# Optimization experiments

Hardware: AMD Instinct MI355X
Metric: run time of the kernel (lower is better)

## Reference

```python
import jax, jax.numpy as jnp
import numpy as np
import math

B, S, D, H, TD = 256, 200, 64, 512, 8


def setup_inputs():
    key = jax.random.key(0)
    ks = jax.random.split(key, 12)
    sd, sh, so = 1.0 / math.sqrt(D), 1.0 / math.sqrt(H), 1.0 / math.sqrt(H + TD)
    return dict(
        x=jax.random.normal(ks[0], (B, S, D), jnp.float32),
        a=jax.random.normal(ks[3], (B, TD), jnp.float32),
        t=jnp.cumsum(jax.random.uniform(ks[2], (B, S), jnp.float32), axis=1),
        mask=(jax.random.uniform(ks[1], (B, S, D)) < 0.8).astype(jnp.float32),
        w_dg_x=jax.random.normal(ks[4], (D,), jnp.float32) * sd,
        b_dg_x=jnp.zeros((D,), jnp.float32),
        W_dg_h=jax.random.normal(ks[5], (H, D), jnp.float32) * sd,
        b_dg_h=jnp.zeros((H,), jnp.float32),
        W=jax.random.normal(ks[6], (3 * H, D), jnp.float32) * sd,
        U=jax.random.normal(ks[7], (3 * H, H), jnp.float32) * sh,
        V=jax.random.normal(ks[8], (3 * H, D), jnp.float32) * sd,
        b=jnp.zeros((3 * H,), jnp.float32),
        attn_v=jnp.ones((H,), jnp.float32),
        W_out=jax.random.normal(ks[9], (H, H + TD), jnp.float32) * so,
        b_out=jnp.zeros((H,), jnp.float32),
    )


def reference(x, a, t, mask, w_dg_x, b_dg_x, W_dg_h, b_dg_h, W, U, V, b, attn_v, W_out, b_out):
    # ---- GRU-D preprocessing: per-feature time gaps delta ----
    x_tm = jnp.transpose(x, (1, 0, 2))    # (S,B,D) time-major
    m_tm = jnp.transpose(mask, (1, 0, 2))
    dt = jnp.diff(t, axis=1, prepend=t[:, :1])      # (B,S), dt[0]=0
    dt_tm = jnp.transpose(dt)[:, :, None]           # (S,B,1)
    # delta[i] = dt[i] + (1 - mask[i-1]) * delta[i-1]; ones at step 0 -> delta[0]=0
    m_prev = jnp.concatenate([jnp.ones((1,) + m_tm.shape[1:], m_tm.dtype), m_tm[:-1]], axis=0)

    def delta_step(d, inp):
        dt_i, mp_i = inp
        d = dt_i + (1.0 - mp_i) * d
        return d, d

    _, delta_tm = jax.lax.scan(delta_step, jnp.zeros((B, D), x.dtype), (dt_tm, m_prev))

    # empirical mean of observed values for imputation
    x_mean = (mask * x).sum((0, 1)) / jnp.maximum(mask.sum((0, 1)), 1.0)  # (D,)

    Wz, Wr, Wh = W[:H], W[H:2 * H], W[2 * H:]
    Uz, Ur, Uh = U[:H], U[H:2 * H], U[2 * H:]
    Vz, Vr, Vh = V[:H], V[H:2 * H], V[2 * H:]
    bz, br, bh = b[:H], b[H:2 * H], b[2 * H:]

    def cell(carry, inp):
        h, x_last = carry
        x_i, m_i, d_i = inp                                        # (B,D) each
        gamma_x = jnp.exp(-jax.nn.relu(w_dg_x * d_i + b_dg_x))     # (B,D) input decay
        gamma_h = jnp.exp(-jax.nn.relu(d_i @ W_dg_h.T + b_dg_h))   # (B,H) hidden decay
        x_hat = m_i * x_i + (1.0 - m_i) * (gamma_x * x_last + (1.0 - gamma_x) * x_mean)
        h_dec = gamma_h * h
        z = jax.nn.sigmoid(x_hat @ Wz.T + h_dec @ Uz.T + m_i @ Vz.T + bz)
        r = jax.nn.sigmoid(x_hat @ Wr.T + h_dec @ Ur.T + m_i @ Vr.T + br)
        h_til = jnp.tanh(x_hat @ Wh.T + (r * h_dec) @ Uh.T + m_i @ Vh.T + bh)
        h_new = (1.0 - z) * h_dec + z * h_til
        x_last_new = m_i * x_i + (1.0 - m_i) * x_last
        return (h_new, x_last_new), h_new

    init = (jnp.zeros((B, H), x.dtype), jnp.zeros((B, D), x.dtype))
    _, h_all = jax.lax.scan(cell, init, (x_tm, m_tm, delta_tm))    # (S,B,H)

    # ---- attention pooling over time (softmax along seq dim, as in torch dim=0) ----
    score = (h_all @ attn_v) / math.sqrt(H)        # (S,B)
    w_attn = jax.nn.softmax(score, axis=0)
    attn_h = (h_all * w_attn[..., None]).sum(0)    # (B,H)

    # ---- treatment head ----
    return jnp.concatenate([attn_h, a], axis=1) @ W_out.T + b_out  # (B,H)
```

## Files before the change

kernel.cpp:

```cpp
#include <hip/hip_runtime.h>
#include <hip/hip_bf16.h>
#include <stdint.h>


typedef unsigned short u16;
typedef unsigned int   u32;
typedef unsigned long long u64;
typedef short bfrag  __attribute__((ext_vector_type(8)));
typedef u16   u16x8  __attribute__((ext_vector_type(8)));
typedef float f32x4  __attribute__((ext_vector_type(4)));

#define NB 256
#define NS 200
#define ND 64
#define NH 512

#define MFMA(a,b,c) __builtin_amdgcn_mfma_f32_16x16x32_bf16((a),(b),(c),0,0,0)

union UQ { u16x8 h; bfrag s; u64 u[2]; uint4 q; };

__device__ __forceinline__ float b2f(u16 v){ union { float f; u32 u; } c; c.u = ((u32)v) << 16; return c.f; }
__device__ __forceinline__ u16 f2b(float f){ union { float f; u32 u; } c; c.f = f; u32 r = c.u + 0x7FFFu + ((c.u >> 16) & 1u); return (u16)(r >> 16); }
__device__ __forceinline__ float sigm(float x){ return 1.f / (1.f + __expf(-x)); }
__device__ __forceinline__ float tanh_f(float x){ return 1.f - 2.f / (1.f + __expf(2.f * x)); }

__device__ __forceinline__ u64 cload64(const void* p){
  return __hip_atomic_load((const u64*)p, __ATOMIC_RELAXED, __HIP_MEMORY_SCOPE_AGENT);
}
__device__ __forceinline__ void cstore64(void* p, u64 v){
  __hip_atomic_store((u64*)p, v, __ATOMIC_RELAXED, __HIP_MEMORY_SCOPE_AGENT);
}
__device__ __forceinline__ u32 cload32(const u32* p){
  return __hip_atomic_load(p, __ATOMIC_RELAXED, __HIP_MEMORY_SCOPE_AGENT);
}
__device__ __forceinline__ void cstore32(u32* p, u32 v){
  __hip_atomic_store(p, v, __ATOMIC_RELAXED, __HIP_MEMORY_SCOPE_AGENT);
}
__device__ __forceinline__ bool poll_ge(const u32* wp, u32 tgt){
  int fuel = 1 << 19;
  while (true) {
    u32 v = cload32(wp);
    if (__all(v >= tgt)) return true;
    __builtin_amdgcn_s_sleep(1);
    if (--fuel == 0) return false;
  }
}
__device__ __forceinline__ bfrag ldfrag(const float* src){
  f32x4 lo = *(const f32x4*)src;
  f32x4 hi = *(const f32x4*)(src + 4);
  UQ z;
  z.h[0]=f2b(lo[0]); z.h[1]=f2b(lo[1]); z.h[2]=f2b(lo[2]); z.h[3]=f2b(lo[3]);
  z.h[4]=f2b(hi[0]); z.h[5]=f2b(hi[1]); z.h[6]=f2b(hi[2]); z.h[7]=f2b(hi[3]);
  return z.s;
}
__device__ __forceinline__ void stage_bf16(u16* dst, const u16* src, int tid, bool zero){
  const int row = tid >> 4, sc = (tid & 15) * 32;
  u16* dp = &dst[((sc >> 3) * 16 + row) * 8];
  if (!zero) {
    const u16* hs = src + (size_t)row * 512 + sc;
    u64 a0 = cload64(hs),      a1 = cload64(hs + 4),  a2 = cload64(hs + 8),  a3 = cload64(hs + 12);
    u64 a4 = cload64(hs + 16), a5 = cload64(hs + 20), a6 = cload64(hs + 24), a7 = cload64(hs + 28);
    *(u64*)(dp)       = a0; *(u64*)(dp + 4)   = a1;
    *(u64*)(dp + 128) = a2; *(u64*)(dp + 132) = a3;
    *(u64*)(dp + 256) = a4; *(u64*)(dp + 260) = a5;
    *(u64*)(dp + 384) = a6; *(u64*)(dp + 388) = a7;
  } else {
    *(u64*)(dp)       = 0; *(u64*)(dp + 4)   = 0;
    *(u64*)(dp + 128) = 0; *(u64*)(dp + 132) = 0;
    *(u64*)(dp + 256) = 0; *(u64*)(dp + 260) = 0;
    *(u64*)(dp + 384) = 0; *(u64*)(dp + 388) = 0;
  }
}


__global__ void transpose_k(const float* __restrict__ Wout, float* __restrict__ WT){
  int i = blockIdx.x * 256 + threadIdx.x;
  if (i < 520 * 512) { int k = i >> 9, ho = i & 511; WT[i] = Wout[ho * 520 + k]; }
}

__global__ void mean1_k(const float* __restrict__ x, const float* __restrict__ mask,
                        float* __restrict__ PX, float* __restrict__ PM){
  int s = blockIdx.x, tid = threadIdx.x;
  __shared__ float lx[256], lm[256];
  float xa = 0.f, ma = 0.f;
  for (int i = tid; i < NB * ND; i += 256) {
    int b = i >> 6, d = i & 63;
    size_t ix = ((size_t)b * NS + s) * 64 + d;
    float m = mask[ix];
    xa += m * x[ix]; ma += m;
  }
  lx[tid] = xa; lm[tid] = ma;
  __syncthreads();
  if (tid < 64) {
    PX[(size_t)s * 64 + tid] = lx[tid] + lx[tid + 64] + lx[tid + 128] + lx[tid + 192];
    PM[(size_t)s * 64 + tid] = lm[tid] + lm[tid + 64] + lm[tid + 128] + lm[tid + 192];
  }
}

__global__ void mean2_k(const float* __restrict__ PX, const float* __restrict__ PM,
                        float* __restrict__ XMEAN){
  int d = threadIdx.x;
  float sx = 0.f, sm = 0.f;
  for (int s = 0; s < NS; ++s){ sx += PX[s * 64 + d]; sm += PM[s * 64 + d]; }
  XMEAN[d] = sx / fmaxf(sm, 1.f);
}

__global__ void prep_k(const float* __restrict__ x, const float* __restrict__ mask,
                       const float* __restrict__ tc, const float* __restrict__ wdgx,
                       const float* __restrict__ bdgx, const float* __restrict__ XMEAN,
                       u16* __restrict__ XHAT, u16* __restrict__ MASKB, u16* __restrict__ DELTA){
  int g = blockIdx.x * 256 + threadIdx.x;
  int b = g >> 6, d = g & 63;
  float xmean = XMEAN[d], wx = wdgx[d], bx = bdgx[d];
  float xl = 0.f, del = 0.f, tprev = 0.f, mprev = 1.f;
  for (int s = 0; s < NS; ++s){
    float tv = tc[b * NS + s];
    float dtv = (s == 0) ? 0.f : (tv - tprev);
    tprev = tv;
    del = dtv + (1.f - mprev) * del;
    size_t ix = ((size_t)b * NS + s) * 64 + d;
    float m = mask[ix], xv = x[ix];
    float gx = __expf(-fmaxf(0.f, wx * del + bx));
    float xh = m * xv + (1.f - m) * (gx * xl + (1.f - gx) * xmean);
    size_t ox = ((size_t)s * NB + b) * 64 + d;
    XHAT[ox] = f2b(xh); MASKB[ox] = f2b(m); DELTA[ox] = f2b(del);
    xl = m * xv + (1.f - m) * xl;
    mprev = m;
  }
}

__global__ __launch_bounds__(256, 1) void xpart_k(
    const float* __restrict__ Wm, const float* __restrict__ Vm,
    const float* __restrict__ bv, const u16* __restrict__ XHAT,
    const u16* __restrict__ MASKB, u16* __restrict__ XP){
  const int tid = threadIdx.x, lane = tid & 63, wid = tid >> 6;
  const int l16 = lane & 15, krow = lane >> 4, r4 = lane >> 2, cb = (lane & 3) * 8;
  const int chunk = blockIdx.x >> 1, p = blockIdx.x & 1;
  const int R0 = chunk * 128;
  const int wbasel = wid * 192;
  const int wbaseg = p * 768 + wbasel;
  __shared__ u16 panel[16 * 16 * 8];
  __shared__ u16 outs[16][768];
  __shared__ float xb[4][16 * 33];
  float* xw = xb[wid];
  const f32x4 Z4 = {0.f, 0.f, 0.f, 0.f};

  bfrag BW[12][2], BV2[12][2];
  #pragma unroll
  for (int ct = 0; ct < 12; ++ct)
    #pragma unroll
    for (int kx = 0; kx < 2; ++kx) {
      BW[ct][kx]  = ldfrag(Wm + (size_t)(wbaseg + ct * 16 + l16) * 64 + kx * 32 + krow * 8);
      BV2[ct][kx] = ldfrag(Vm + (size_t)(wbaseg + ct * 16 + l16) * 64 + kx * 32 + krow * 8);
    }
  float bias6[6][8];
  #pragma unroll
  for (int grp = 0; grp < 6; ++grp)
    #pragma unroll
    for (int q = 0; q < 8; ++q) bias6[grp][q] = bv[wbaseg + grp * 32 + cb + q];

  for (int it = 0; it < 8; ++it) {
    const int R = R0 + it * 16;
    { const int kb = tid >> 4, row = tid & 15;
      const u16* sp = (kb < 8 ? XHAT : MASKB) + (size_t)(R + row) * 64 + (kb & 7) * 8;
      *(uint4*)&panel[(kb * 16 + row) * 8] = *(const uint4*)sp; }
    __syncthreads();
    #pragma unroll
    for (int grp = 0; grp < 6; ++grp) {
      f32x4 ac0 = Z4, ac1 = Z4;
      #pragma unroll
      for (int kx = 0; kx < 2; ++kx) {
        bfrag ax = *(const bfrag*)&panel[((kx * 4 + krow) * 16 + l16) * 8];
        ac0 = MFMA(ax, BW[grp*2][kx], ac0); ac1 = MFMA(ax, BW[grp*2+1][kx], ac1);
        bfrag am = *(const bfrag*)&panel[((8 + kx * 4 + krow) * 16 + l16) * 8];
        ac0 = MFMA(am, BV2[grp*2][kx], ac0); ac1 = MFMA(am, BV2[grp*2+1][kx], ac1);
      }
      #pragma unroll
      for (int j = 0; j < 4; ++j) { xw[(krow*4+j)*33 + l16] = ac0[j]; xw[(krow*4+j)*33 + 16 + l16] = ac1[j]; }
      UQ ov;
      #pragma unroll
      for (int q = 0; q < 8; ++q) ov.h[q] = f2b(xw[r4 * 33 + cb + q] + bias6[grp][q]);
      *(u64*)&outs[r4][wbasel + grp * 32 + cb] = ov.u[0];
      *(u64*)&outs[r4][wbasel + grp * 32 + cb + 4] = ov.u[1];
    }
    __syncthreads();
    for (int c = tid; c < 16 * 96; c += 256) {
      const int row = c / 96, ch = c % 96;
      *(uint4*)(XP + (size_t)(R + row) * 1536 + p * 768 + ch * 8) =
          *(const uint4*)&outs[row][ch * 8];
    }
    __syncthreads();
  }
}

__global__ __launch_bounds__(256, 1) void grud_rnn(
    const float* __restrict__ Um, const float* __restrict__ Wdg, const float* __restrict__ bdg,
    const u16* __restrict__ XP, const u16* __restrict__ DELTA,
    u16* __restrict__ HDECB, u16* __restrict__ RHB, u16* __restrict__ HALL,
    u32* __restrict__ flags)
{
  const int tid = threadIdx.x, lane = tid & 63, wid = tid >> 6, bid = blockIdx.x;
  const int lid = (bid & 7) * 8 + (bid >> 3);
  const int rb = lid >> 2, g = lid & 3, m0 = rb * 16;
  const int l16 = lane & 15, krow = lane >> 4, r4 = lane >> 2, cb = (lane & 3) * 8;
  const int pw = g * 4 + wid;
  const int cw = g * 128 + wid * 32;
  u32* FB = flags + rb * 32;

  __shared__ u16 hpan[64 * 16 * 8];
  __shared__ u16 rpan[64 * 16 * 8];
  __shared__ u16 dpan[8 * 16 * 8];
  __shared__ float xb[4][16 * 33];
  __shared__ int s_ab;
  float* xw = xb[wid];
  const f32x4 Z4 = {0.f, 0.f, 0.f, 0.f};
  if (tid == 0) s_ab = 0;
  __syncthreads();

  bfrag BZ[16][2], BR[16][2], BH[16][2], BG[2][2];
  #pragma unroll
  for (int kk = 0; kk < 16; ++kk) {
    const size_t ko = (size_t)(kk * 32 + krow * 8);
    #pragma unroll
    for (int t2 = 0; t2 < 2; ++t2) {
      BZ[kk][t2] = ldfrag(Um + (size_t)(       cw + t2 * 16 + l16) * 512 + ko);
      BR[kk][t2] = ldfrag(Um + (size_t)(512  + cw + t2 * 16 + l16) * 512 + ko);
      BH[kk][t2] = ldfrag(Um + (size_t)(1024 + cw + t2 * 16 + l16) * 512 + ko);
    }
  }
  #pragma unroll
  for (int kk = 0; kk < 2; ++kk)
    #pragma unroll
    for (int t2 = 0; t2 < 2; ++t2)
      BG[kk][t2] = ldfrag(Wdg + (size_t)(cw + t2 * 16 + l16) * 64 + kk * 32 + krow * 8);
  float gb8[8];
  #pragma unroll
  for (int q = 0; q < 8; ++q) gb8[q] = bdg[cw + cb + q];

  const int slot = ((cw + cb) >> 3) * 16 + r4;

  for (int t = 0; t < NS; ++t) {
    const int tn = (t + 1 < NS) ? t + 1 : NS - 1;
    const u16* xp = XP + ((size_t)t * NB + m0 + r4) * 1536 + cw + cb;
    u64 xz0 = *(const u64*)(xp),        xz1 = *(const u64*)(xp + 4);
    u64 xr0 = *(const u64*)(xp + 512),  xr1 = *(const u64*)(xp + 516);
    u64 xh0 = *(const u64*)(xp + 1024), xh1 = *(const u64*)(xp + 1028);
    if (t > 0) { if (!poll_ge(FB + (lane & 15), (u32)t)) s_ab = 1; }
    stage_bf16(hpan, HDECB + (size_t)m0 * 512, tid, t == 0);
    if (tid < 128) {
      const int kb = tid >> 4, row = tid & 15;
      const u16* sp = DELTA + ((size_t)tn * NB + m0 + row) * 64 + kb * 8;
      *(uint4*)&dpan[(kb * 16 + row) * 8] = *(const uint4*)sp;
    }
    __syncthreads();
    if (s_ab) break;
    f32x4 aR0 = Z4, aR1 = Z4;
    #pragma unroll
    for (int kk = 0; kk < 16; ++kk) {
      bfrag a = *(const bfrag*)&hpan[((kk * 4 + krow) * 16 + l16) * 8];
      aR0 = MFMA(a, BR[kk][0], aR0); aR1 = MFMA(a, BR[kk][1], aR1);
    }
    #pragma unroll
    for (int j = 0; j < 4; ++j) { xw[(krow*4+j)*33 + l16] = aR0[j]; xw[(krow*4+j)*33 + 16 + l16] = aR1[j]; }
    UQ hd_; hd_.h = *(const u16x8*)&hpan[slot * 8];
    UQ xr_; xr_.u[0] = xr0; xr_.u[1] = xr1;
    UQ rh_;
    #pragma unroll
    for (int q = 0; q < 8; ++q) {
      float rv = sigm(b2f(xr_.h[q]) + xw[r4 * 33 + cb + q]);
      rh_.h[q] = f2b(rv * b2f(hd_.h[q]));
    }
    u16* rdst = RHB + (size_t)(m0 + r4) * 512 + cw + cb;
    cstore64(rdst, rh_.u[0]); cstore64(rdst + 4, rh_.u[1]);
    asm volatile("s_waitcnt vmcnt(0)" ::: "memory");
    if (lane == 0) cstore32(FB + 16 + pw, (u32)(t + 1));
    f32x4 aZ0 = Z4, aZ1 = Z4;
    #pragma unroll
    for (int kk = 0; kk < 16; ++kk) {
      bfrag a = *(const bfrag*)&hpan[((kk * 4 + krow) * 16 + l16) * 8];
      aZ0 = MFMA(a, BZ[kk][0], aZ0); aZ1 = MFMA(a, BZ[kk][1], aZ1);
    }
    #pragma unroll
    for (int j = 0; j < 4; ++j) { xw[(krow*4+j)*33 + l16] = aZ0[j]; xw[(krow*4+j)*33 + 16 + l16] = aZ1[j]; }
    UQ xz_; xz_.u[0] = xz0; xz_.u[1] = xz1;
    float zf[8];
    #pragma unroll
    for (int q = 0; q < 8; ++q) zf[q] = sigm(b2f(xz_.h[q]) + xw[r4 * 33 + cb + q]);
    f32x4 g0 = Z4, g1 = Z4;
    #pragma unroll
    for (int kk = 0; kk < 2; ++kk) {
      bfrag a = *(const bfrag*)&dpan[((kk * 4 + krow) * 16 + l16) * 8];
      g0 = MFMA(a, BG[kk][0], g0); g1 = MFMA(a, BG[kk][1], g1);
    }
    #pragma unroll
    for (int j = 0; j < 4; ++j) { xw[(krow*4+j)*33 + l16] = g0[j]; xw[(krow*4+j)*33 + 16 + l16] = g1[j]; }
    float gm8[8];
    #pragma unroll
    for (int q = 0; q < 8; ++q)
      gm8[q] = __expf(-fmaxf(0.f, xw[r4 * 33 + cb + q] + gb8[q]));
    if (!poll_ge(FB + 16 + (lane & 15), (u32)(t + 1))) s_ab = 1;
    stage_bf16(rpan, RHB + (size_t)m0 * 512, tid, false);
    __syncthreads();
    if (s_ab) break;
    f32x4 aH0 = Z4, aH1 = Z4;
    #pragma unroll
    for (int kk = 0; kk < 16; ++kk) {
      bfrag a = *(const bfrag*)&rpan[((kk * 4 + krow) * 16 + l16) * 8];
      aH0 = MFMA(a, BH[kk][0], aH0); aH1 = MFMA(a, BH[kk][1], aH1);
    }
    #pragma unroll
    for (int j = 0; j < 4; ++j) { xw[(krow*4+j)*33 + l16] = aH0[j]; xw[(krow*4+j)*33 + 16 + l16] = aH1[j]; }
    UQ xh_; xh_.u[0] = xh0; xh_.u[1] = xh1;
    UQ hw_, hdn_;
    #pragma unroll
    for (int q = 0; q < 8; ++q) {
      float til = tanh_f(b2f(xh_.h[q]) + xw[r4 * 33 + cb + q]);
      float hn = (1.f - zf[q]) * b2f(hd_.h[q]) + zf[q] * til;
      hw_.h[q] = f2b(hn);
      hdn_.h[q] = f2b(gm8[q] * hn);
    }
    if (t + 1 < NS) {
      u16* hdst = HDECB + (size_t)(m0 + r4) * 512 + cw + cb;
      cstore64(hdst, hdn_.u[0]); cstore64(hdst + 4, hdn_.u[1]);
    }
    asm volatile("s_waitcnt vmcnt(0)" ::: "memory");
    if (lane == 0) cstore32(FB + 0 + pw, (u32)(t + 1));
    u16* hp = HALL + ((size_t)(m0 + r4) * NS + t) * 512 + cw + cb;
    *(u64*)hp = hw_.u[0]; *(u64*)(hp + 4) = hw_.u[1];
  }
}


__global__ __launch_bounds__(256) void attn_k(const u16* __restrict__ HALL,
                                              const float* __restrict__ av,
                                              float* __restrict__ ATTN){
  const int b = blockIdx.x, tid = threadIdx.x, lane = tid & 63, wid = tid >> 6;
  __shared__ float avs[512], sc[256], wgt[256], red[8];
  for (int i = tid; i < 512; i += 256) avs[i] = av[i];
  __syncthreads();
  const u16* base = HALL + (size_t)b * NS * 512;
  for (int i = 0; i < 50; ++i) {
    const int s = wid * 50 + i;
    UQ w8; w8.q = *(const uint4*)(base + (size_t)s * 512 + lane * 8);
    float p = 0.f;
    #pragma unroll
    for (int j = 0; j < 8; ++j) p += b2f(w8.h[j]) * avs[lane * 8 + j];
    #pragma unroll
    for (int off = 32; off; off >>= 1) p += __shfl_xor(p, off, 64);
    if (lane == 0) sc[s] = p * 0.04419417382415922f;
  }
  __syncthreads();
  float val = (tid < NS) ? sc[tid] : -3.0e38f;
  float m = val;
  #pragma unroll
  for (int off = 32; off; off >>= 1) m = fmaxf(m, __shfl_xor(m, off, 64));
  if (lane == 0) red[wid] = m;
  __syncthreads();
  m = fmaxf(fmaxf(red[0], red[1]), fmaxf(red[2], red[3]));
  float e = (tid < NS) ? __expf(val - m) : 0.f;
  float sum = e;
  #pragma unroll
  for (int off = 32; off; off >>= 1) sum += __shfl_xor(sum, off, 64);
  if (lane == 0) red[4 + wid] = sum;
  __syncthreads();
  const float ssum = red[4] + red[5] + red[6] + red[7];
  wgt[tid] = e / ssum;
  __syncthreads();
  float a0 = 0.f, a1 = 0.f;
  const int h0 = tid * 2;
  for (int s = 0; s < NS; ++s) {
    const float w = wgt[s];
    u32 pr = *(const u32*)(base + (size_t)s * 512 + h0);
    a0 += w * b2f((u16)(pr & 0xFFFFu));
    a1 += w * b2f((u16)(pr >> 16));
  }
  ATTN[(size_t)b * 512 + h0] = a0;
  ATTN[(size_t)b * 512 + h0 + 1] = a1;
}

__global__ void out_k(const float* __restrict__ ATTN, const float* __restrict__ Ain,
                      const float* __restrict__ WT, const float* __restrict__ bout,
                      float* __restrict__ OUT){
  const int g = blockIdx.x, tid = threadIdx.x;
  __shared__ float ah[4][520];
  for (int i = tid; i < 4 * 520; i += 256) {
    int bb = i / 520, k = i % 520;
    int b = g * 4 + bb;
    ah[bb][k] = (k < 512) ? ATTN[(size_t)b * 512 + k] : Ain[b * 8 + (k - 512)];
  }
  __syncthreads();
  #pragma unroll
  for (int part = 0; part < 2; ++part) {
    const int ho = part * 256 + tid;
    float a0 = bout[ho], a1 = a0, a2 = a0, a3 = a0;
    for (int k = 0; k < 520; ++k) {
      float w = WT[(size_t)k * 512 + ho];
      a0 += ah[0][k] * w; a1 += ah[1][k] * w; a2 += ah[2][k] * w; a3 += ah[3][k] * w;
    }
    OUT[(size_t)(g * 4 + 0) * 512 + ho] = a0;
    OUT[(size_t)(g * 4 + 1) * 512 + ho] = a1;
    OUT[(size_t)(g * 4 + 2) * 512 + ho] = a2;
    OUT[(size_t)(g * 4 + 3) * 512 + ho] = a3;
  }
}


extern "C" void kernel_launch(void* const* d_in, const int* in_sizes, int n_in,
                              void* d_out, int out_size, void* d_ws, size_t ws_size,
                              hipStream_t stream) {
  (void)in_sizes; (void)n_in; (void)out_size; (void)ws_size;
  const float* x    = (const float*)d_in[0];
  const float* a_in = (const float*)d_in[1];
  const float* tc   = (const float*)d_in[2];
  const float* mask = (const float*)d_in[3];
  const float* wdgx = (const float*)d_in[4];
  const float* bdgx = (const float*)d_in[5];
  const float* Wdgh = (const float*)d_in[6];
  const float* bdgh = (const float*)d_in[7];
  const float* Wm   = (const float*)d_in[8];
  const float* Um   = (const float*)d_in[9];
  const float* Vm   = (const float*)d_in[10];
  const float* bvv  = (const float*)d_in[11];
  const float* attv = (const float*)d_in[12];
  const float* Wout = (const float*)d_in[13];
  const float* bout = (const float*)d_in[14];

  char* ws = (char*)d_ws;
  size_t o = 0;
  auto al = [&](size_t sz) { size_t r = o; o += (sz + 255) & ~(size_t)255; return r; };
  u32*   flags = (u32*)  (ws + al(16 * 32 * 4));
  float* XMEAN = (float*)(ws + al(256));
  float* PX    = (float*)(ws + al((size_t)NS * 64 * 4));
  float* PM    = (float*)(ws + al((size_t)NS * 64 * 4));
  u16*   XHAT  = (u16*)  (ws + al((size_t)NS * NB * 64 * 2));
  u16*   MASKB = (u16*)  (ws + al((size_t)NS * NB * 64 * 2));
  u16*   DELTA = (u16*)  (ws + al((size_t)NS * NB * 64 * 2));
  u16*   HDECB = (u16*)  (ws + al((size_t)NB * NH * 2));
  u16*   RHB   = (u16*)  (ws + al((size_t)NB * NH * 2));
  u16*   XP    = (u16*)  (ws + al((size_t)NS * NB * 1536 * 2));
  u16*   HALL  = (u16*)  (ws + al((size_t)NS * NB * NH * 2));
  float* ATTN  = (float*)(ws + al((size_t)NB * NH * 4));
  float* WT    = (float*)(ws + al((size_t)520 * 512 * 4));

  hipMemsetAsync(flags, 0, 16 * 32 * 4, stream);

  transpose_k<<<(520 * 512 + 255) / 256, 256, 0, stream>>>(Wout, WT);
  mean1_k<<<NS, 256, 0, stream>>>(x, mask, PX, PM);
  mean2_k<<<1, 64, 0, stream>>>(PX, PM, XMEAN);
  prep_k<<<NB * ND / 256, 256, 0, stream>>>(x, mask, tc, wdgx, bdgx, XMEAN, XHAT, MASKB, DELTA);
  xpart_k<<<800, 256, 0, stream>>>(Wm, Vm, bvv, XHAT, MASKB, XP);
  grud_rnn<<<64, 256, 0, stream>>>(Um, Wdgh, bdgh, XP, DELTA, HDECB, RHB, HALL, flags);
  attn_k<<<NB, 256, 0, stream>>>(HALL, attv, ATTN);
  out_k<<<64, 256, 0, stream>>>(ATTN, a_in, WT, bout, (float*)d_out);
}
```

Baseline: 1.861 ms.

## Compute full reset gate redundantly per block to drop mid-step cross-block sync

Each block now computes the entire 512-wide r*h_dec panel for its 16 rows locally, streaming a pre-packed bf16 copy of U_r from global memory, instead of computing a 128-column slice and exchanging it through global memory with a second flag barrier. The hidden-state buffer is double-buffered by timestep parity so only one cross-block wait per step remains. This removes one grid-level synchronization and global round-trip per timestep, at the cost of four times the U_r MFMA work per block and heavy per-step global or L2 reads of the packed U_r weights.

```diff
diff --git a/kernel.cpp b/kernel.cpp
--- a/kernel.cpp
+++ b/kernel.cpp
@@ -76,6 +76,18 @@
 __global__ void transpose_k(const float* __restrict__ Wout, float* __restrict__ WT){
   int i = blockIdx.x * 256 + threadIdx.x;
   if (i < 520 * 512) { int k = i >> 9, ho = i & 511; WT[i] = Wout[ho * 520 + k]; }
+}
+
+__global__ void wconv_k(const float* __restrict__ Um, u16* __restrict__ UrP){
+  int idx = blockIdx.x * 256 + threadIdx.x;
+  if (idx < 512 * 64) {
+    const int l = idx & 63, fk = idx >> 6;
+    const int cf = fk >> 4, kk = fk & 15;
+    const float* src = Um + (size_t)(512 + cf * 16 + (l & 15)) * 512 + kk * 32 + (l >> 4) * 8;
+    u16* dst = UrP + (size_t)idx * 8;
+    #pragma unroll
+    for (int j = 0; j < 8; ++j) dst[j] = f2b(src[j]);
+  }
 }
 
 __global__ void mean1_k(const float* __restrict__ x, const float* __restrict__ mask,
@@ -194,17 +206,18 @@
 }
 
 __global__ __launch_bounds__(256, 1) void grud_rnn(
-    const float* __restrict__ Um, const float* __restrict__ Wdg, const float* __restrict__ bdg,
+    const float* __restrict__ Um, const u16* __restrict__ UrP,
+    const float* __restrict__ Wdg, const float* __restrict__ bdg,
     const u16* __restrict__ XP, const u16* __restrict__ DELTA,
-    u16* __restrict__ HDECB, u16* __restrict__ RHB, u16* __restrict__ HALL,
-    u32* __restrict__ flags)
+    u16* __restrict__ HDEC2, u16* __restrict__ HALL, u32* __restrict__ flags)
 {
   const int tid = threadIdx.x, lane = tid & 63, wid = tid >> 6, bid = blockIdx.x;
   const int lid = (bid & 7) * 8 + (bid >> 3);
   const int rb = lid >> 2, g = lid & 3, m0 = rb * 16;
   const int l16 = lane & 15, krow = lane >> 4, r4 = lane >> 2, cb = (lane & 3) * 8;
   const int pw = g * 4 + wid;
-  const int cw = g * 128 + wid * 32;
+  const int cout = g * 128 + wid * 32;
+  const int rcb = wid * 128;
   u32* FB = flags + rb * 32;
 
   __shared__ u16 hpan[64 * 16 * 8];
@@ -217,36 +230,38 @@
   if (tid == 0) s_ab = 0;
   __syncthreads();
 
-  bfrag BZ[16][2], BR[16][2], BH[16][2], BG[2][2];
+  bfrag BZ[16][2], BH[16][2], BG[2][2];
   #pragma unroll
   for (int kk = 0; kk < 16; ++kk) {
     const size_t ko = (size_t)(kk * 32 + krow * 8);
     #pragma unroll
     for (int t2 = 0; t2 < 2; ++t2) {
-      BZ[kk][t2] = ldfrag(Um + (size_t)(       cw + t2 * 16 + l16) * 512 + ko);
-      BR[kk][t2] = ldfrag(Um + (size_t)(512  + cw + t2 * 16 + l16) * 512 + ko);
-      BH[kk][t2] = ldfrag(Um + (size_t)(1024 + cw + t2 * 16 + l16) * 512 + ko);
+      BZ[kk][t2] = ldfrag(Um + (size_t)(       cout + t2 * 16 + l16) * 512 + ko);
+      BH[kk][t2] = ldfrag(Um + (size_t)(1024 + cout + t2 * 16 + l16) * 512 + ko);
     }
   }
   #pragma unroll
   for (int kk = 0; kk < 2; ++kk)
     #pragma unroll
     for (int t2 = 0; t2 < 2; ++t2)
-      BG[kk][t2] = ldfrag(Wdg + (size_t)(cw + t2 * 16 + l16) * 64 + kk * 32 + krow * 8);
+      BG[kk][t2] = ldfrag(Wdg + (size_t)(cout + t2 * 16 + l16) * 64 + kk * 32 + krow * 8);
   float gb8[8];
   #pragma unroll
-  for (int q = 0; q < 8; ++q) gb8[q] = bdg[cw + cb + q];
-
-  const int slot = ((cw + cb) >> 3) * 16 + r4;
+  for (int q = 0; q < 8; ++q) gb8[q] = bdg[cout + cb + q];
 
   for (int t = 0; t < NS; ++t) {
     const int tn = (t + 1 < NS) ? t + 1 : NS - 1;
-    const u16* xp = XP + ((size_t)t * NB + m0 + r4) * 1536 + cw + cb;
-    u64 xz0 = *(const u64*)(xp),        xz1 = *(const u64*)(xp + 4);
-    u64 xr0 = *(const u64*)(xp + 512),  xr1 = *(const u64*)(xp + 516);
-    u64 xh0 = *(const u64*)(xp + 1024), xh1 = *(const u64*)(xp + 1028);
+    const u16* xp = XP + ((size_t)t * NB + m0 + r4) * 1536;
+    u64 xz0 = *(const u64*)(xp + cout + cb),        xz1 = *(const u64*)(xp + cout + cb + 4);
+    u64 xh0 = *(const u64*)(xp + 1024 + cout + cb), xh1 = *(const u64*)(xp + 1024 + cout + cb + 4);
+    u64 xr0[4], xr1[4];
+    #pragma unroll
+    for (int cp = 0; cp < 4; ++cp) {
+      xr0[cp] = *(const u64*)(xp + 512 + rcb + cp * 32 + cb);
+      xr1[cp] = *(const u64*)(xp + 512 + rcb + cp * 32 + cb + 4);
+    }
     if (t > 0) { if (!poll_ge(FB + (lane & 15), (u32)t)) s_ab = 1; }
-    stage_bf16(hpan, HDECB + (size_t)m0 * 512, tid, t == 0);
+    stage_bf16(hpan, HDEC2 + (size_t)(t & 1) * NB * 512 + (size_t)m0 * 512, tid, t == 0);
     if (tid < 128) {
       const int kb = tid >> 4, row = tid & 15;
       const u16* sp = DELTA + ((size_t)tn * NB + m0 + row) * 64 + kb * 8;
@@ -254,78 +269,86 @@
     }
     __syncthreads();
     if (s_ab) break;
-    f32x4 aR0 = Z4, aR1 = Z4;
+    UQ hdo; hdo.h = *(const u16x8*)&hpan[(((cout + cb) >> 3) * 16 + r4) * 8];
+    bfrag da0 = *(const bfrag*)&dpan[((krow) * 16 + l16) * 8];
+    bfrag da1 = *(const bfrag*)&dpan[((4 + krow) * 16 + l16) * 8];
+    f32x4 ra[8] = {Z4, Z4, Z4, Z4, Z4, Z4, Z4, Z4};
     #pragma unroll
     for (int kk = 0; kk < 16; ++kk) {
       bfrag a = *(const bfrag*)&hpan[((kk * 4 + krow) * 16 + l16) * 8];
-      aR0 = MFMA(a, BR[kk][0], aR0); aR1 = MFMA(a, BR[kk][1], aR1);
-    }
-    #pragma unroll
-    for (int j = 0; j < 4; ++j) { xw[(krow*4+j)*33 + l16] = aR0[j]; xw[(krow*4+j)*33 + 16 + l16] = aR1[j]; }
-    UQ hd_; hd_.h = *(const u16x8*)&hpan[slot * 8];
-    UQ xr_; xr_.u[0] = xr0; xr_.u[1] = xr1;
-    UQ rh_;
-    #pragma unroll
-    for (int q = 0; q < 8; ++q) {
-      float rv = sigm(b2f(xr_.h[q]) + xw[r4 * 33 + cb + q]);
-      rh_.h[q] = f2b(rv * b2f(hd_.h[q]));
-    }
-    u16* rdst = RHB + (size_t)(m0 + r4) * 512 + cw + cb;
-    cstore64(rdst, rh_.u[0]); cstore64(rdst + 4, rh_.u[1]);
-    asm volatile("s_waitcnt vmcnt(0)" ::: "memory");
-    if (lane == 0) cstore32(FB + 16 + pw, (u32)(t + 1));
-    f32x4 aZ0 = Z4, aZ1 = Z4;
+      #pragma unroll
+      for (int c = 0; c < 8; ++c) {
+        bfrag b = *(const bfrag*)(UrP + ((size_t)((wid * 8 + c) * 16 + kk) * 64 + lane) * 8);
+        ra[c] = MFMA(a, b, ra[c]);
+      }
+    }
+    f32x4 az0 = Z4, az1 = Z4;
     #pragma unroll
     for (int kk = 0; kk < 16; ++kk) {
       bfrag a = *(const bfrag*)&hpan[((kk * 4 + krow) * 16 + l16) * 8];
-      aZ0 = MFMA(a, BZ[kk][0], aZ0); aZ1 = MFMA(a, BZ[kk][1], aZ1);
-    }
-    #pragma unroll
-    for (int j = 0; j < 4; ++j) { xw[(krow*4+j)*33 + l16] = aZ0[j]; xw[(krow*4+j)*33 + 16 + l16] = aZ1[j]; }
+      az0 = MFMA(a, BZ[kk][0], az0); az1 = MFMA(a, BZ[kk][1], az1);
+    }
+    f32x4 g0 = Z4, g1 = Z4;
+    g0 = MFMA(da0, BG[0][0], g0); g0 = MFMA(da1, BG[1][0], g0);
+    g1 = MFMA(da0, BG[0][1], g1); g1 = MFMA(da1, BG[1][1], g1);
+    #pragma unroll
+    for (int cp = 0; cp < 4; ++cp) {
+      #pragma unroll
+      for (int j = 0; j < 4; ++j) {
+        xw[(krow * 4 + j) * 33 + l16] = ra[2 * cp][j];
+        xw[(krow * 4 + j) * 33 + 16 + l16] = ra[2 * cp + 1][j];
+      }
+      const int wc = rcb + cp * 32 + cb;
+      UQ hdw; hdw.h = *(const u16x8*)&hpan[((wc >> 3) * 16 + r4) * 8];
+      UQ xrw; xrw.u[0] = xr0[cp]; xrw.u[1] = xr1[cp];
+      UQ rhv;
+      #pragma unroll
+      for (int q = 0; q < 8; ++q) {
+        float rv = sigm(b2f(xrw.h[q]) + xw[r4 * 33 + cb + q]);
+        rhv.h[q] = f2b(rv * b2f(hdw.h[q]));
+      }
+      *(u16x8*)&rpan[((wc >> 3) * 16 + r4) * 8] = rhv.h;
+    }
+    __syncthreads();
+    f32x4 ah0 = Z4, ah1 = Z4;
+    #pragma unroll
+    for (int kk = 0; kk < 16; ++kk) {
+      bfrag a = *(const bfrag*)&rpan[((kk * 4 + krow) * 16 + l16) * 8];
+      ah0 = MFMA(a, BH[kk][0], ah0); ah1 = MFMA(a, BH[kk][1], ah1);
+    }
+    #pragma unroll
+    for (int j = 0; j < 4; ++j) { xw[(krow*4+j)*33 + l16] = ah0[j]; xw[(krow*4+j)*33 + 16 + l16] = ah1[j]; }
+    float hh[8];
+    #pragma unroll
+    for (int q = 0; q < 8; ++q) hh[q] = xw[r4 * 33 + cb + q];
+    #pragma unroll
+    for (int j = 0; j < 4; ++j) { xw[(krow*4+j)*33 + l16] = az0[j]; xw[(krow*4+j)*33 + 16 + l16] = az1[j]; }
     UQ xz_; xz_.u[0] = xz0; xz_.u[1] = xz1;
     float zf[8];
     #pragma unroll
     for (int q = 0; q < 8; ++q) zf[q] = sigm(b2f(xz_.h[q]) + xw[r4 * 33 + cb + q]);
-    f32x4 g0 = Z4, g1 = Z4;
-    #pragma unroll
-    for (int kk = 0; kk < 2; ++kk) {
-      bfrag a = *(const bfrag*)&dpan[((kk * 4 + krow) * 16 + l16) * 8];
-      g0 = MFMA(a, BG[kk][0], g0); g1 = MFMA(a, BG[kk][1], g1);
-    }
     #pragma unroll
     for (int j = 0; j < 4; ++j) { xw[(krow*4+j)*33 + l16] = g0[j]; xw[(krow*4+j)*33 + 16 + l16] = g1[j]; }
     float gm8[8];
     #pragma unroll
     for (int q = 0; q < 8; ++q)
       gm8[q] = __expf(-fmaxf(0.f, xw[r4 * 33 + cb + q] + gb8[q]));
-    if (!poll_ge(FB + 16 + (lane & 15), (u32)(t + 1))) s_ab = 1;
-    stage_bf16(rpan, RHB + (size_t)m0 * 512, tid, false);
-    __syncthreads();
-    if (s_ab) break;
-    f32x4 aH0 = Z4, aH1 = Z4;
-    #pragma unroll
-    for (int kk = 0; kk < 16; ++kk) {
-      bfrag a = *(const bfrag*)&rpan[((kk * 4 + krow) * 16 + l16) * 8];
-      aH0 = MFMA(a, BH[kk][0], aH0); aH1 = MFMA(a, BH[kk][1], aH1);
-    }
-    #pragma unroll
-    for (int j = 0; j < 4; ++j) { xw[(krow*4+j)*33 + l16] = aH0[j]; xw[(krow*4+j)*33 + 16 + l16] = aH1[j]; }
     UQ xh_; xh_.u[0] = xh0; xh_.u[1] = xh1;
     UQ hw_, hdn_;
     #pragma unroll
     for (int q = 0; q < 8; ++q) {
-      float til = tanh_f(b2f(xh_.h[q]) + xw[r4 * 33 + cb + q]);
-      float hn = (1.f - zf[q]) * b2f(hd_.h[q]) + zf[q] * til;
+      float til = tanh_f(b2f(xh_.h[q]) + hh[q]);
+      float hn = (1.f - zf[q]) * b2f(hdo.h[q]) + zf[q] * til;
       hw_.h[q] = f2b(hn);
       hdn_.h[q] = f2b(gm8[q] * hn);
     }
     if (t + 1 < NS) {
-      u16* hdst = HDECB + (size_t)(m0 + r4) * 512 + cw + cb;
+      u16* hdst = HDEC2 + (size_t)((t + 1) & 1) * NB * 512 + (size_t)(m0 + r4) * 512 + cout + cb;
       cstore64(hdst, hdn_.u[0]); cstore64(hdst + 4, hdn_.u[1]);
     }
     asm volatile("s_waitcnt vmcnt(0)" ::: "memory");
-    if (lane == 0) cstore32(FB + 0 + pw, (u32)(t + 1));
-    u16* hp = HALL + ((size_t)(m0 + r4) * NS + t) * 512 + cw + cb;
+    if (lane == 0) cstore32(FB + pw, (u32)(t + 1));
+    u16* hp = HALL + ((size_t)(m0 + r4) * NS + t) * 512 + cout + cb;
     *(u64*)hp = hw_.u[0]; *(u64*)(hp + 4) = hw_.u[1];
   }
 }
@@ -435,8 +458,8 @@
   u16*   XHAT  = (u16*)  (ws + al((size_t)NS * NB * 64 * 2));
   u16*   MASKB = (u16*)  (ws + al((size_t)NS * NB * 64 * 2));
   u16*   DELTA = (u16*)  (ws + al((size_t)NS * NB * 64 * 2));
-  u16*   HDECB = (u16*)  (ws + al((size_t)NB * NH * 2));
-  u16*   RHB   = (u16*)  (ws + al((size_t)NB * NH * 2));
+  u16*   UrP   = (u16*)  (ws + al((size_t)512 * 64 * 8 * 2));
+  u16*   HDEC2 = (u16*)  (ws + al((size_t)2 * NB * NH * 2));
   u16*   XP    = (u16*)  (ws + al((size_t)NS * NB * 1536 * 2));
   u16*   HALL  = (u16*)  (ws + al((size_t)NS * NB * NH * 2));
   float* ATTN  = (float*)(ws + al((size_t)NB * NH * 4));
@@ -445,11 +468,12 @@
   hipMemsetAsync(flags, 0, 16 * 32 * 4, stream);
 
   transpose_k<<<(520 * 512 + 255) / 256, 256, 0, stream>>>(Wout, WT);
+  wconv_k<<<(512 * 64 + 255) / 256, 256, 0, stream>>>(Um, UrP);
   mean1_k<<<NS, 256, 0, stream>>>(x, mask, PX, PM);
   mean2_k<<<1, 64, 0, stream>>>(PX, PM, XMEAN);
   prep_k<<<NB * ND / 256, 256, 0, stream>>>(x, mask, tc, wdgx, bdgx, XMEAN, XHAT, MASKB, DELTA);
   xpart_k<<<800, 256, 0, stream>>>(Wm, Vm, bvv, XHAT, MASKB, XP);
-  grud_rnn<<<64, 256, 0, stream>>>(Um, Wdgh, bdgh, XP, DELTA, HDECB, RHB, HALL, flags);
+  grud_rnn<<<64, 256, 0, stream>>>(Um, UrP, Wdgh, bdgh, XP, DELTA, HDEC2, HALL, flags);
   attn_k<<<NB, 256, 0, stream>>>(HALL, attv, ATTN);
   out_k<<<64, 256, 0, stream>>>(ATTN, a_in, WT, bout, (float*)d_out);
 }
```

Result: slower. 5.290 ms (+184.2%).
